# Performance work log

Measured on AMD Instinct MI355X. Metric: run time of the kernel, lower is better.

The kernel has to match this reference:

```python
import jax, jax.numpy as jnp
import numpy as np

L, D, H, B, S, V = 4, 1024, 16, 8, 512, 32000
DK = D // H          # per-head dim = 64; only head 0 is ever used (bug in source)
FF = 4 * D
EPS = 1e-3           # keras BatchNormalization default epsilon


def _bn(x, gamma, beta, mean, var):
    # inference-mode BatchNorm over last axis (keras default)
    return gamma * (x - mean) * jax.lax.rsqrt(var + EPS) + beta


def setup_inputs() -> dict:
    key = jax.random.key(0)
    keys = iter(jax.random.split(key, 40))

    def rn(shape, scale=0.02):
        return jax.random.normal(next(keys), shape, jnp.float32) * scale

    sequence = jax.random.randint(next(keys), (B, S), 0, V, dtype=jnp.int32)

    # standard sinusoidal positional encoding table [S, D]
    pos = np.arange(S)[:, None].astype(np.float32)
    i = np.arange(D)[None, :]
    angle = pos / np.power(10000.0, (2 * (i // 2)) / D).astype(np.float32)
    pes = np.where(i % 2 == 0, np.sin(angle), np.cos(angle)).astype(np.float32)

    return {
        "sequence": sequence,
        "emb": rn((V, D)),
        "pes": jnp.asarray(pes),
        # single-head attention params (head 0 only, per the source bug), stacked over layers
        "wq": rn((L, D, DK)), "bq": jnp.zeros((L, DK)),
        "wk": rn((L, D, DK)), "bk": jnp.zeros((L, DK)),
        "wv": rn((L, D, DK)), "bv": jnp.zeros((L, DK)),
        "wo": rn((L, DK, D)), "bo": jnp.zeros((L, D)),
        "att_gamma": 1.0 + rn((L, D), 0.1), "att_beta": rn((L, D), 0.1),
        "att_mean": rn((L, D), 0.1), "att_var": jnp.ones((L, D)),
        "w1": rn((L, D, FF)), "bff1": jnp.zeros((L, FF)),
        "w2": rn((L, FF, D)), "bff2": jnp.zeros((L, D)),
        "ffn_gamma": 1.0 + rn((L, D), 0.1), "ffn_beta": rn((L, D), 0.1),
        "ffn_mean": rn((L, D), 0.1), "ffn_var": jnp.ones((L, D)),
    }


def reference(sequence, emb, pes, wq, bq, wk, bk, wv, bv, wo, bo,
              att_gamma, att_beta, att_mean, att_var,
              w1, bff1, w2, bff2,
              ffn_gamma, ffn_beta, ffn_mean, ffn_var):
    # embedding + positional bug: only pes[i, 0] (a scalar per position) is added
    x = emb[sequence] + pes[:S, 0:1][None]          # [B, S, D]
    scale = 1.0 / jnp.sqrt(jnp.float32(DK))
    for l in range(L):
        q = x @ wq[l] + bq[l]                       # [B, S, DK]
        k = x @ wk[l] + bk[l]
        v = x @ wv[l] + bv[l]
        score = jnp.einsum('bqd,bkd->bqk', q, k) * scale
        head = jax.nn.softmax(score, axis=-1) @ v   # [B, S, DK]
        att = head @ wo[l] + bo[l]                  # [B, S, D]
        x = _bn(x + att, att_gamma[l], att_beta[l], att_mean[l], att_var[l])
        ffn = jax.nn.relu(x @ w1[l] + bff1[l]) @ w2[l] + bff2[l]
        x = _bn(x + ffn, ffn_gamma[l], ffn_beta[l], ffn_mean[l], ffn_var[l])
    return x
```

## Files before the change

### kernel.cpp

```cpp
#include <hip/hip_runtime.h>
#include <hip/hip_bf16.h>
#include <stdint.h>

#define L_  4
#define D_  1024
#define DK_ 64
#define B_  8
#define S_  512
#define FF_ 4096
#define M_  (B_*S_)
#define EPS_ 1e-3f
#define QKVN_ 256

typedef __bf16 bf16_t;
typedef bf16_t bf16x8 __attribute__((ext_vector_type(8)));
typedef float  f32x4  __attribute__((ext_vector_type(4)));

__device__ __forceinline__ bf16_t f2b(float f) {
    union { float f; uint32_t u; } v; v.f = f;
    uint32_t r = v.u + 0x7fff + ((v.u >> 16) & 1);
    uint16_t h = (uint16_t)(r >> 16);
    bf16_t o; __builtin_memcpy(&o, &h, 2); return o;
}

__device__ __forceinline__ void gl2lds16(const bf16_t* g, bf16_t* l) {
    __builtin_amdgcn_global_load_lds(
        (__attribute__((address_space(1))) void*)g,
        (__attribute__((address_space(3))) void*)l, 16, 0, 0);
}

__global__ void embed_kernel(const int* __restrict__ seq, const float* __restrict__ emb,
                             const float* __restrict__ pes, float* __restrict__ x,
                             bf16_t* __restrict__ xb) {
    int idx = blockIdx.x * 256 + threadIdx.x;
    int md  = idx >> 10;
    int d   = idx & (D_ - 1);
    int s   = md & (S_ - 1);
    float v = emb[(size_t)seq[md] * D_ + d] + pes[s * D_];
    x[idx] = v;
    xb[idx] = f2b(v);
}

__device__ __forceinline__ void tile_tr(const float* __restrict__ src, bf16_t* __restrict__ dst,
                                        int K, int N, int kb, int nb, float (*t)[33]) {
    int k0 = kb * 32, n0 = nb * 32;
    int c = threadIdx.x & 31, r = threadIdx.x >> 5;
    #pragma unroll
    for (int i = 0; i < 4; i++)
        t[r + i * 8][c] = src[(size_t)(k0 + r + i * 8) * N + n0 + c];
    __syncthreads();
    #pragma unroll
    for (int i = 0; i < 4; i++)
        dst[(size_t)(n0 + r + i * 8) * K + k0 + c] = f2b(t[c][r + i * 8]);
}

__global__ void prep_weights(const float* __restrict__ wq, const float* __restrict__ wk,
                             const float* __restrict__ wv, const float* __restrict__ wo,
                             const float* __restrict__ w1, const float* __restrict__ w2,
                             const float* __restrict__ bq, const float* __restrict__ bk,
                             const float* __restrict__ bv,
                             bf16_t* __restrict__ wqkvt, bf16_t* __restrict__ wot,
                             bf16_t* __restrict__ w1t, bf16_t* __restrict__ w2t,
                             float* __restrict__ bqkv) {
    __shared__ float t[32][33];
    int bid = blockIdx.x;
    if (bid < 4096) {
        tile_tr(w1, w1t, D_, FF_, bid & 31, bid >> 5, t);
    } else if (bid < 8192) {
        int rem = bid - 4096;
        tile_tr(w2, w2t, FF_, D_, rem & 127, rem >> 7, t);
    } else if (bid < 8384) {
        int rem = bid - 8192;
        int which = rem >> 6; rem &= 63;
        const float* src = which == 0 ? wq : (which == 1 ? wk : wv);
        tile_tr(src, wqkvt + (size_t)which * 64 * D_, D_, DK_, rem & 31, rem >> 5, t);
    } else if (bid < 8448) {
        int rem = bid - 8384;
        tile_tr(wo, wot, DK_, D_, rem & 1, rem >> 1, t);
    } else if (bid < 8464) {
        int rem = bid - 8448;
        bf16_t* z = wqkvt + (size_t)192 * D_ + rem * 4096;
        for (int i = threadIdx.x; i < 4096; i += 256) z[i] = (bf16_t)0.f;
    } else {
        int n = threadIdx.x;
        float v = 0.f;
        if      (n <  64) v = bq[n];
        else if (n < 128) v = bk[n - 64];
        else if (n < 192) v = bv[n - 128];
        bqkv[n] = v;
    }
}

template<int MODE>
__global__ __launch_bounds__(256)
void gemm_mfma3(const bf16_t* __restrict__ A, const bf16_t* __restrict__ Bt,
                const float* __restrict__ bias, bf16_t* __restrict__ Cb,
                const float* __restrict__ Xin, float* __restrict__ Xf, bf16_t* __restrict__ Xb,
                const float* __restrict__ g, const float* __restrict__ bb,
                const float* __restrict__ mu, const float* __restrict__ var,
                int N, int K, int kChunk, size_t strideZ) {
    __shared__ bf16_t As[128 * 64];
    __shared__ bf16_t Bs[128 * 64];
    const int tid  = threadIdx.x;
    const int w    = tid >> 6, lane = tid & 63;
    const int wm   = w >> 1,   wn   = w & 1;
    const int lm   = lane & 15, quad = lane >> 4;
    const int m0 = blockIdx.y * 128, n0 = blockIdx.x * 128;
    const int kBeg = blockIdx.z * kChunk, kEnd = kBeg + kChunk;
    const int lrow = lane >> 3;
    const int lk   = (lane & 7) ^ lrow;

    f32x4 acc[4][4];
    #pragma unroll
    for (int i = 0; i < 4; i++)
        #pragma unroll
        for (int j = 0; j < 4; j++) acc[i][j] = (f32x4){0.f, 0.f, 0.f, 0.f};

    for (int k0 = kBeg; k0 < kEnd; k0 += 64) {
        #pragma unroll
        for (int i = 0; i < 4; i++) {
            const int r0 = w * 32 + i * 8;
            gl2lds16(A  + (size_t)(m0 + r0 + lrow) * K + k0 + lk * 8, As + r0 * 64);
            gl2lds16(Bt + (size_t)(n0 + r0 + lrow) * K + k0 + lk * 8, Bs + r0 * 64);
        }
        __syncthreads();
        #pragma unroll
        for (int s = 0; s < 2; s++) {
            bf16x8 af[4], bfr[4];
            #pragma unroll
            for (int mi = 0; mi < 4; mi++) {
                const int ra = wm * 64 + mi * 16 + lm;
                af[mi] = *(const bf16x8*)(As + ra * 64 + (((s * 4 + quad) ^ (lm & 7)) * 8));
            }
            #pragma unroll
            for (int ni = 0; ni < 4; ni++) {
                const int rb = wn * 64 + ni * 16 + lm;
                bfr[ni] = *(const bf16x8*)(Bs + rb * 64 + (((s * 4 + quad) ^ (lm & 7)) * 8));
            }
            #pragma unroll
            for (int mi = 0; mi < 4; mi++)
                #pragma unroll
                for (int ni = 0; ni < 4; ni++)
                    acc[mi][ni] = __builtin_amdgcn_mfma_f32_16x16x32_bf16(
                        af[mi], bfr[ni], acc[mi][ni], 0, 0, 0);
        }
        __syncthreads();
    }

    bf16_t* Pz = (MODE == 2) ? Cb + (size_t)blockIdx.z * strideZ : Cb;

    #pragma unroll
    for (int ni = 0; ni < 4; ni++) {
        const int col = n0 + wn * 64 + ni * 16 + lm;
        float bv = 0.f, gv = 0.f, bbv = 0.f, muv = 0.f, rsv = 0.f;
        if (MODE != 2) bv = bias[col];
        if (MODE == 3) {
            gv = g[col]; bbv = bb[col]; muv = mu[col];
            rsv = rsqrtf(var[col] + EPS_);
        }
        #pragma unroll
        for (int mi = 0; mi < 4; mi++) {
            const int rbase = m0 + wm * 64 + mi * 16 + quad * 4;
            #pragma unroll
            for (int r = 0; r < 4; r++) {
                const size_t idx = (size_t)(rbase + r) * N + col;
                float v = acc[mi][ni][r] + bv;
                if (MODE == 2) Pz[idx] = f2b(v);
                if (MODE == 3) {
                    float s = Xin[idx] + v;
                    float o = gv * (s - muv) * rsv + bbv;
                    Xf[idx] = o;
                    Xb[idx] = f2b(o);
                }
            }
        }
    }
}

template<int MODE>
__global__ __launch_bounds__(512, 2)
void gemm_8ph(const bf16_t* __restrict__ A, const bf16_t* __restrict__ Bt,
              const float* __restrict__ bias, bf16_t* __restrict__ Cb,
              int N, int K, int kChunk, size_t strideZ) {
    __shared__ bf16_t As[2][256 * 64];
    __shared__ bf16_t Bs[2][256 * 64];
    const int tid  = threadIdx.x;
    const int w    = tid >> 6, lane = tid & 63;
    const int wm   = w >> 2,   wn   = w & 3;
    const int lm   = lane & 15, quad = lane >> 4;
    const int m0 = blockIdx.y * 256, n0 = blockIdx.x * 256;
    const int kBeg = blockIdx.z * kChunk;
    const int lrow = lane >> 3;
    const int lk   = (lane & 7) ^ lrow;
    const int niter = kChunk >> 7;

    f32x4 acc[8][4];
    #pragma unroll
    for (int i = 0; i < 8; i++)
        #pragma unroll
        for (int j = 0; j < 4; j++) acc[i][j] = (f32x4){0.f, 0.f, 0.f, 0.f};

    auto stageA = [&](int buf, int half, int tile) {
        const int kt0 = kBeg + tile * 64;
        #pragma unroll
        for (int j = 0; j < 2; j++) {
            const int r0 = half * 128 + w * 16 + j * 8;
            gl2lds16(A + (size_t)(m0 + r0 + lrow) * K + kt0 + lk * 8, &As[buf][r0 * 64]);
        }
    };
    auto stageB = [&](int buf, int half, int tile) {
        const int kt0 = kBeg + tile * 64;
        #pragma unroll
        for (int j = 0; j < 2; j++) {
            const int r0 = half * 128 + w * 16 + j * 8;
            gl2lds16(Bt + (size_t)(n0 + r0 + lrow) * K + kt0 + lk * 8, &Bs[buf][r0 * 64]);
        }
    };

    bf16x8 af[8], bfr[4];
    auto ldFrags = [&](int buf, int kk) {
        #pragma unroll
        for (int mi = 0; mi < 8; mi++) {
            const int ra = wm * 128 + mi * 16 + lm;
            af[mi] = *(const bf16x8*)(&As[buf][ra * 64 + (((kk * 4 + quad) ^ (lm & 7)) * 8)]);
        }
        #pragma unroll
        for (int ni = 0; ni < 4; ni++) {
            const int rb = wn * 64 + ni * 16 + lm;
            bfr[ni] = *(const bf16x8*)(&Bs[buf][rb * 64 + (((kk * 4 + quad) ^ (lm & 7)) * 8)]);
        }
    };
    auto mfmaHalf = [&](int mh) {
        __builtin_amdgcn_s_setprio(1);
        #pragma unroll
        for (int mi = mh * 4; mi < mh * 4 + 4; mi++)
            #pragma unroll
            for (int ni = 0; ni < 4; ni++)
                acc[mi][ni] = __builtin_amdgcn_mfma_f32_16x16x32_bf16(
                    af[mi], bfr[ni], acc[mi][ni], 0, 0, 0);
        __builtin_amdgcn_s_setprio(0);
    };

    stageA(0, 0, 0); stageA(0, 1, 0); stageB(0, 0, 0); stageB(0, 1, 0);
    stageA(1, 0, 1);
    asm volatile("s_waitcnt vmcnt(2)" ::: "memory");
    __builtin_amdgcn_sched_barrier(0);
    __builtin_amdgcn_s_barrier();

    for (int i = 0; i < niter; i++) {
        const int t0 = 2 * i;
        const bool nl = (i < niter - 1);
        ldFrags(0, 0);
        stageA(1, 1, t0 + 1);
        __builtin_amdgcn_s_barrier();
        mfmaHalf(0);
        __builtin_amdgcn_s_barrier();
        stageB(1, 0, t0 + 1);
        __builtin_amdgcn_s_barrier();
        mfmaHalf(1);
        __builtin_amdgcn_s_barrier();
        ldFrags(0, 1);
        stageB(1, 1, t0 + 1);
        __builtin_amdgcn_s_barrier();
        mfmaHalf(0);
        __builtin_amdgcn_s_barrier();
        if (nl) {
            stageA(0, 0, t0 + 2);
            asm volatile("s_waitcnt vmcnt(2)" ::: "memory");
        } else {
            asm volatile("s_waitcnt vmcnt(0)" ::: "memory");
        }
        __builtin_amdgcn_sched_barrier(0);
        __builtin_amdgcn_s_barrier();
        mfmaHalf(1);
        __builtin_amdgcn_s_barrier();
        ldFrags(1, 0);
        if (nl) stageA(0, 1, t0 + 2);
        __builtin_amdgcn_s_barrier();
        mfmaHalf(0);
        __builtin_amdgcn_s_barrier();
        if (nl) stageB(0, 0, t0 + 2);
        __builtin_amdgcn_s_barrier();
        mfmaHalf(1);
        __builtin_amdgcn_s_barrier();
        ldFrags(1, 1);
        if (nl) stageB(0, 1, t0 + 2);
        __builtin_amdgcn_s_barrier();
        mfmaHalf(0);
        __builtin_amdgcn_s_barrier();
        if (nl) {
            stageA(1, 0, t0 + 3);
            asm volatile("s_waitcnt vmcnt(2)" ::: "memory");
        } else {
            asm volatile("s_waitcnt vmcnt(0)" ::: "memory");
        }
        __builtin_amdgcn_sched_barrier(0);
        __builtin_amdgcn_s_barrier();
        mfmaHalf(1);
        __builtin_amdgcn_s_barrier();
    }

    bf16_t* Pz = (MODE == 2) ? Cb + (size_t)blockIdx.z * strideZ : Cb;

    #pragma unroll
    for (int ni = 0; ni < 4; ni++) {
        const int col = n0 + wn * 64 + ni * 16 + lm;
        float bv = 0.f;
        if (MODE == 1) bv = bias[col];
        #pragma unroll
        for (int mi = 0; mi < 8; mi++) {
            const int rbase = m0 + wm * 128 + mi * 16 + quad * 4;
            #pragma unroll
            for (int r = 0; r < 4; r++) {
                const size_t idx = (size_t)(rbase + r) * N + col;
                float v = acc[mi][ni][r] + bv;
                if (MODE == 1) Cb[idx] = f2b(fmaxf(v, 0.f));
                if (MODE == 2) Pz[idx] = f2b(v);
            }
        }
    }
}

__global__ void qkv_reduce(const bf16_t* __restrict__ P, const float* __restrict__ bias,
                           bf16_t* __restrict__ dst) {
    int idx = blockIdx.x * 256 + threadIdx.x;
    int n = idx & (QKVN_ - 1);
    float s = bias[n];
    #pragma unroll
    for (int zz = 0; zz < 4; zz++) s += (float)P[(size_t)zz * M_ * QKVN_ + idx];
    dst[idx] = f2b(s);
}

__global__ void vt_kernel(const bf16_t* __restrict__ qkv, bf16_t* __restrict__ Vt) {
    int b = blockIdx.y, k0 = blockIdx.x * 64;
    const bf16_t* vb = qkv + (size_t)b * S_ * QKVN_ + 128;
    __shared__ bf16_t t[64][65];
    int c = threadIdx.x & 63, r4 = threadIdx.x >> 6;
    #pragma unroll
    for (int i = 0; i < 16; i++) {
        int k = i * 4 + r4;
        t[c][k] = vb[(size_t)(k0 + k) * QKVN_ + c];
    }
    __syncthreads();
    #pragma unroll
    for (int i = 0; i < 16; i++) {
        int d = i * 4 + r4;
        Vt[((size_t)b * DK_ + d) * S_ + k0 + c] = t[d][c];
    }
}

__global__ __launch_bounds__(256)
void attn_fused(const bf16_t* __restrict__ qkv, const bf16_t* __restrict__ Vt,
                bf16_t* __restrict__ hdb) {
    const int b  = blockIdx.y;
    const int i0 = blockIdx.x * 64;
    const bf16_t* qb  = qkv + (size_t)b * S_ * QKVN_;
    const bf16_t* kb  = qb + 64;
    const bf16_t* vtb = Vt + (size_t)b * DK_ * S_;

    __shared__ bf16_t Ps[8 * 64 * 64];
    __shared__ bf16_t Vs[8 * 64 * 64];
    __shared__ float  rowred[4][64];

    const int tid  = threadIdx.x;
    const int w    = tid >> 6, lane = tid & 63;
    const int lm   = lane & 15, quad = lane >> 4;
    const int lrow = lane >> 3;
    const int lk   = (lane & 7) ^ lrow;

    #pragma unroll
    for (int i = 0; i < 16; i++) {
        const int r0 = w * 16 + (i & 1) * 8;
        const int kt = i >> 1;
        gl2lds16(vtb + (size_t)(r0 + lrow) * S_ + kt * 64 + lk * 8,
                 Vs + kt * 4096 + r0 * 64);
    }

    f32x4 acc[4][8];
    #pragma unroll
    for (int mi = 0; mi < 4; mi++)
        #pragma unroll
        for (int ni = 0; ni < 8; ni++) acc[mi][ni] = (f32x4){0.f, 0.f, 0.f, 0.f};

    #pragma unroll
    for (int s = 0; s < 2; s++) {
        bf16x8 af[4], bfr[8];
        #pragma unroll
        for (int mi = 0; mi < 4; mi++)
            af[mi] = *(const bf16x8*)(qb + (size_t)(i0 + mi * 16 + lm) * QKVN_ + s * 32 + quad * 8);
        #pragma unroll
        for (int ni = 0; ni < 8; ni++)
            bfr[ni] = *(const bf16x8*)(kb + (size_t)(w * 128 + ni * 16 + lm) * QKVN_ + s * 32 + quad * 8);
        #pragma unroll
        for (int mi = 0; mi < 4; mi++)
            #pragma unroll
            for (int ni = 0; ni < 8; ni++)
                acc[mi][ni] = __builtin_amdgcn_mfma_f32_16x16x32_bf16(
                    af[mi], bfr[ni], acc[mi][ni], 0, 0, 0);
    }
    #pragma unroll
    for (int mi = 0; mi < 4; mi++)
        #pragma unroll
        for (int ni = 0; ni < 8; ni++) acc[mi][ni] *= 0.125f;

    float rmax[4][4];
    #pragma unroll
    for (int mi = 0; mi < 4; mi++)
        #pragma unroll
        for (int r = 0; r < 4; r++) {
            float m = acc[mi][0][r];
            #pragma unroll
            for (int ni = 1; ni < 8; ni++) m = fmaxf(m, acc[mi][ni][r]);
            #pragma unroll
            for (int off = 1; off < 16; off <<= 1) m = fmaxf(m, __shfl_xor(m, off, 64));
            rmax[mi][r] = m;
        }
    if (lm == 0) {
        #pragma unroll
        for (int mi = 0; mi < 4; mi++)
            #pragma unroll
            for (int r = 0; r < 4; r++)
                rowred[w][mi * 16 + quad * 4 + r] = rmax[mi][r];
    }
    __syncthreads();
    float gmax[4][4];
    #pragma unroll
    for (int mi = 0; mi < 4; mi++)
        #pragma unroll
        for (int r = 0; r < 4; r++) {
            const int row = mi * 16 + quad * 4 + r;
            gmax[mi][r] = fmaxf(fmaxf(rowred[0][row], rowred[1][row]),
                                fmaxf(rowred[2][row], rowred[3][row]));
        }
    __syncthreads();

    float rsum[4][4];
    #pragma unroll
    for (int mi = 0; mi < 4; mi++)
        #pragma unroll
        for (int r = 0; r < 4; r++) rsum[mi][r] = 0.f;
    #pragma unroll
    for (int mi = 0; mi < 4; mi++) {
        #pragma unroll
        for (int ni = 0; ni < 8; ni++) {
            const int key = w * 128 + ni * 16 + lm;
            const int kt  = key >> 6;
            const int ck  = (key >> 3) & 7;
            #pragma unroll
            for (int r = 0; r < 4; r++) {
                const int m = mi * 16 + quad * 4 + r;
                float p = __expf(acc[mi][ni][r] - gmax[mi][r]);
                bf16_t pb = f2b(p);
                rsum[mi][r] += (float)pb;
                Ps[kt * 4096 + m * 64 + ((ck ^ (m & 7)) * 8) + (key & 7)] = pb;
            }
        }
    }
    #pragma unroll
    for (int mi = 0; mi < 4; mi++)
        #pragma unroll
        for (int r = 0; r < 4; r++) {
            float s = rsum[mi][r];
            #pragma unroll
            for (int off = 1; off < 16; off <<= 1) s += __shfl_xor(s, off, 64);
            rsum[mi][r] = s;
        }
    if (lm == 0) {
        #pragma unroll
        for (int mi = 0; mi < 4; mi++)
            #pragma unroll
            for (int r = 0; r < 4; r++)
                rowred[w][mi * 16 + quad * 4 + r] = rsum[mi][r];
    }
    __syncthreads();

    f32x4 accO[4];
    #pragma unroll
    for (int ni = 0; ni < 4; ni++) accO[ni] = (f32x4){0.f, 0.f, 0.f, 0.f};
    #pragma unroll
    for (int ks = 0; ks < 16; ks++) {
        const int kt = ks >> 1;
        const int co = (ks & 1) * 4 + quad;
        bf16x8 af = *(const bf16x8*)(Ps + kt * 4096 + (w * 16 + lm) * 64 + ((co ^ (lm & 7)) * 8));
        #pragma unroll
        for (int ni = 0; ni < 4; ni++) {
            bf16x8 bfr = *(const bf16x8*)(Vs + kt * 4096 + (ni * 16 + lm) * 64 + ((co ^ (lm & 7)) * 8));
            accO[ni] = __builtin_amdgcn_mfma_f32_16x16x32_bf16(af, bfr, accO[ni], 0, 0, 0);
        }
    }

    #pragma unroll
    for (int r = 0; r < 4; r++) {
        const int row = w * 16 + quad * 4 + r;
        const float tot = rowred[0][row] + rowred[1][row] + rowred[2][row] + rowred[3][row];
        const float inv = 1.0f / tot;
        #pragma unroll
        for (int ni = 0; ni < 4; ni++)
            hdb[(size_t)(b * S_ + i0 + row) * DK_ + ni * 16 + lm] = f2b(accO[ni][r] * inv);
    }
}

__global__ void bn_residual4(const float* __restrict__ x, const bf16_t* __restrict__ p,
                             const float* __restrict__ bias,
                             const float* __restrict__ g, const float* __restrict__ b,
                             const float* __restrict__ mu, const float* __restrict__ var,
                             float* __restrict__ dst, bf16_t* __restrict__ dstb) {
    int idx = blockIdx.x * 256 + threadIdx.x;
    int d = idx & (D_ - 1);
    float r = bias[d] + (float)p[idx] + (float)p[(size_t)M_ * D_ + idx]
            + (float)p[2 * (size_t)M_ * D_ + idx] + (float)p[3 * (size_t)M_ * D_ + idx];
    float s = x[idx] + r;
    float o = g[d] * (s - mu[d]) * rsqrtf(var[d] + EPS_) + b[d];
    dst[idx] = o;
    dstb[idx] = f2b(o);
}

extern "C" void kernel_launch(void* const* d_in, const int* in_sizes, int n_in,
                              void* d_out, int out_size, void* d_ws, size_t ws_size,
                              hipStream_t stream) {
    const int*   seq = (const int*)  d_in[0];
    const float* emb = (const float*)d_in[1];
    const float* pes = (const float*)d_in[2];
    const float* wq  = (const float*)d_in[3];
    const float* bq  = (const float*)d_in[4];
    const float* wk  = (const float*)d_in[5];
    const float* bk  = (const float*)d_in[6];
    const float* wv  = (const float*)d_in[7];
    const float* bv  = (const float*)d_in[8];
    const float* wo  = (const float*)d_in[9];
    const float* bo  = (const float*)d_in[10];
    const float* ag  = (const float*)d_in[11];
    const float* ab  = (const float*)d_in[12];
    const float* am  = (const float*)d_in[13];
    const float* av  = (const float*)d_in[14];
    const float* w1  = (const float*)d_in[15];
    const float* b1  = (const float*)d_in[16];
    const float* w2  = (const float*)d_in[17];
    const float* b2  = (const float*)d_in[18];
    const float* fg  = (const float*)d_in[19];
    const float* fb  = (const float*)d_in[20];
    const float* fm  = (const float*)d_in[21];
    const float* fv  = (const float*)d_in[22];
    float* out = (float*)d_out;

    char* p = (char*)d_ws;
    auto alloc = [&](size_t bytes) { char* q = p; p += (bytes + 255) & ~(size_t)255; return q; };
    float*  X     = (float*) alloc((size_t)M_ * D_ * 4);
    bf16_t* Xb    = (bf16_t*)alloc((size_t)M_ * D_ * 2);
    bf16_t* qkvb  = (bf16_t*)alloc((size_t)M_ * QKVN_ * 2);
    bf16_t* Vtb   = (bf16_t*)alloc((size_t)B_ * DK_ * S_ * 2);
    bf16_t* hdb   = (bf16_t*)alloc((size_t)M_ * DK_ * 2);
    bf16_t* hb    = (bf16_t*)alloc((size_t)M_ * FF_ * 2);
    bf16_t* w1t   = (bf16_t*)alloc((size_t)FF_ * D_ * 2);
    bf16_t* w2t   = (bf16_t*)alloc((size_t)D_ * FF_ * 2);
    bf16_t* wqkvt = (bf16_t*)alloc((size_t)QKVN_ * D_ * 2);
    bf16_t* wot   = (bf16_t*)alloc((size_t)D_ * DK_ * 2);
    bf16_t* part  = (bf16_t*)alloc((size_t)4 * M_ * D_ * 2);
    float*  bqkv  = (float*) alloc(QKVN_ * 4);

    embed_kernel<<<M_ * D_ / 256, 256, 0, stream>>>(seq, emb, pes, X, Xb);

    for (int l = 0; l < L_; l++) {
        prep_weights<<<8465, 256, 0, stream>>>(
            wq + (size_t)l * D_ * DK_, wk + (size_t)l * D_ * DK_, wv + (size_t)l * D_ * DK_,
            wo + (size_t)l * DK_ * D_, w1 + (size_t)l * D_ * FF_, w2 + (size_t)l * FF_ * D_,
            bq + l * DK_, bk + l * DK_, bv + l * DK_,
            wqkvt, wot, w1t, w2t, bqkv);

        gemm_mfma3<2><<<dim3(QKVN_ / 128, M_ / 128, 4), 256, 0, stream>>>(
            Xb, wqkvt, nullptr, (bf16_t*)out, nullptr, nullptr, nullptr,
            nullptr, nullptr, nullptr, nullptr, QKVN_, D_, D_ / 4, (size_t)M_ * QKVN_);
        qkv_reduce<<<M_ * QKVN_ / 256, 256, 0, stream>>>((const bf16_t*)out, bqkv, qkvb);

        vt_kernel<<<dim3(S_ / 64, B_), 256, 0, stream>>>(qkvb, Vtb);
        attn_fused<<<dim3(S_ / 64, B_), 256, 0, stream>>>(qkvb, Vtb, hdb);

        gemm_mfma3<3><<<dim3(D_ / 128, M_ / 128, 1), 256, 0, stream>>>(
            hdb, wot, bo + l * D_, nullptr, X, X, Xb,
            ag + l * D_, ab + l * D_, am + l * D_, av + l * D_, D_, DK_, DK_, 0);

        gemm_8ph<1><<<dim3(FF_ / 256, M_ / 256, 1), 512, 0, stream>>>(
            Xb, w1t, b1 + l * FF_, hb, FF_, D_, D_, 0);

        gemm_8ph<2><<<dim3(D_ / 256, M_ / 256, 4), 512, 0, stream>>>(
            hb, w2t, nullptr, part, D_, FF_, FF_ / 4, (size_t)M_ * D_);

        bn_residual4<<<M_ * D_ / 256, 256, 0, stream>>>(
            X, part, b2 + l * D_,
            fg + l * D_, fb + l * D_, fm + l * D_, fv + l * D_, X, Xb);
        if (l == L_ - 1)
            hipMemcpyAsync(out, X, (size_t)M_ * D_ * 4, hipMemcpyDeviceToDevice, stream);
    }
}
```

Baseline: 934.7 us.

## Replace 8-phase GEMM pipeline with 4-stage K32 ring buffer and XCD-aware block remap

The FFN GEMMs drop the hand-interleaved 8-phase schedule with double-buffered K=64 tiles. They now use a 4-deep ring of K=32 LDS tiles, prefetching three tiles ahead with a single barrier per k-step and a different XOR swizzle. Workgroup IDs are also remapped round-robin across the 8 XCDs to improve L2 locality. This trades the finer-grained overlap of loads and MFMAs for deeper prefetch and fewer barriers, but each k-step does less MFMA work per barrier.

New measurement: 989.7 us. +5.9%, slower.

```diff
diff --git a/kernel.cpp b/kernel.cpp
--- a/kernel.cpp
+++ b/kernel.cpp
@@ -179,20 +179,25 @@
 
 template<int MODE>
 __global__ __launch_bounds__(512, 2)
-void gemm_8ph(const bf16_t* __restrict__ A, const bf16_t* __restrict__ Bt,
-              const float* __restrict__ bias, bf16_t* __restrict__ Cb,
-              int N, int K, int kChunk, size_t strideZ) {
-    __shared__ bf16_t As[2][256 * 64];
-    __shared__ bf16_t Bs[2][256 * 64];
+void gemm_ring(const bf16_t* __restrict__ A, const bf16_t* __restrict__ Bt,
+               const float* __restrict__ bias, bf16_t* __restrict__ Cb,
+               int N, int K, int kChunk, size_t strideZ) {
+    __shared__ bf16_t As[4][256 * 32];
+    __shared__ bf16_t Bs[4][256 * 32];
     const int tid  = threadIdx.x;
     const int w    = tid >> 6, lane = tid & 63;
     const int wm   = w >> 2,   wn   = w & 3;
     const int lm   = lane & 15, quad = lane >> 4;
-    const int m0 = blockIdx.y * 256, n0 = blockIdx.x * 256;
+
+    const int nwg = gridDim.x * gridDim.y;
+    int wg = blockIdx.y * gridDim.x + blockIdx.x;
+    wg = (wg & 7) * (nwg >> 3) + (wg >> 3);
+    const int m0 = (wg / gridDim.x) * 256, n0 = (wg % gridDim.x) * 256;
+
     const int kBeg = blockIdx.z * kChunk;
-    const int lrow = lane >> 3;
-    const int lk   = (lane & 7) ^ lrow;
-    const int niter = kChunk >> 7;
+    const int nkt  = kChunk >> 5;
+    const int lrow = lane >> 2;
+    const int lk   = (lane & 3) ^ ((lane >> 3) & 3);
 
     f32x4 acc[8][4];
     #pragma unroll
@@ -200,103 +205,65 @@
         #pragma unroll
         for (int j = 0; j < 4; j++) acc[i][j] = (f32x4){0.f, 0.f, 0.f, 0.f};
 
-    auto stageA = [&](int buf, int half, int tile) {
-        const int kt0 = kBeg + tile * 64;
+    auto stage = [&](const bf16_t* __restrict__ src, int base, int tile, bf16_t* dst) {
+        const int kt0 = kBeg + tile * 32;
         #pragma unroll
         for (int j = 0; j < 2; j++) {
-            const int r0 = half * 128 + w * 16 + j * 8;
-            gl2lds16(A + (size_t)(m0 + r0 + lrow) * K + kt0 + lk * 8, &As[buf][r0 * 64]);
+            const int r0 = w * 32 + j * 16;
+            gl2lds16(src + (size_t)(base + r0 + lrow) * K + kt0 + lk * 8, dst + r0 * 32);
         }
     };
-    auto stageB = [&](int buf, int half, int tile) {
-        const int kt0 = kBeg + tile * 64;
-        #pragma unroll
-        for (int j = 0; j < 2; j++) {
-            const int r0 = half * 128 + w * 16 + j * 8;
-            gl2lds16(Bt + (size_t)(n0 + r0 + lrow) * K + kt0 + lk * 8, &Bs[buf][r0 * 64]);
-        }
-    };
-
-    bf16x8 af[8], bfr[4];
-    auto ldFrags = [&](int buf, int kk) {
-        #pragma unroll
-        for (int mi = 0; mi < 8; mi++) {
+
+    #pragma unroll
+    for (int t = 0; t < 3; t++) {
+        stage(A,  m0, t, As[t]);
+        stage(Bt, n0, t, Bs[t]);
+    }
+
+    for (int kt = 0; kt < nkt; ++kt) {
+        const int buf = kt & 3;
+        if (kt + 3 < nkt) {
+            const int sb = (kt + 3) & 3;
+            stage(A,  m0, kt + 3, As[sb]);
+            stage(Bt, n0, kt + 3, Bs[sb]);
+            asm volatile("s_waitcnt vmcnt(12)" ::: "memory");
+        } else if (kt + 3 == nkt) {
+            asm volatile("s_waitcnt vmcnt(8)" ::: "memory");
+        } else if (kt + 2 == nkt) {
+            asm volatile("s_waitcnt vmcnt(4)" ::: "memory");
+        } else {
+            asm volatile("s_waitcnt vmcnt(0)" ::: "memory");
+        }
+        __builtin_amdgcn_sched_barrier(0);
+        __builtin_amdgcn_s_barrier();
+        __builtin_amdgcn_sched_barrier(0);
+
+        bf16x8 af[8], bfr[4];
+        #pragma unroll
+        for (int mi = 0; mi < 4; mi++) {
             const int ra = wm * 128 + mi * 16 + lm;
-            af[mi] = *(const bf16x8*)(&As[buf][ra * 64 + (((kk * 4 + quad) ^ (lm & 7)) * 8)]);
+            af[mi] = *(const bf16x8*)(&As[buf][ra * 32 + ((quad ^ ((ra >> 1) & 3)) * 8)]);
         }
         #pragma unroll
         for (int ni = 0; ni < 4; ni++) {
             const int rb = wn * 64 + ni * 16 + lm;
-            bfr[ni] = *(const bf16x8*)(&Bs[buf][rb * 64 + (((kk * 4 + quad) ^ (lm & 7)) * 8)]);
-        }
-    };
-    auto mfmaHalf = [&](int mh) {
+            bfr[ni] = *(const bf16x8*)(&Bs[buf][rb * 32 + ((quad ^ ((rb >> 1) & 3)) * 8)]);
+        }
+        #pragma unroll
+        for (int mi = 4; mi < 8; mi++) {
+            const int ra = wm * 128 + mi * 16 + lm;
+            af[mi] = *(const bf16x8*)(&As[buf][ra * 32 + ((quad ^ ((ra >> 1) & 3)) * 8)]);
+        }
+
         __builtin_amdgcn_s_setprio(1);
         #pragma unroll
-        for (int mi = mh * 4; mi < mh * 4 + 4; mi++)
+        for (int mi = 0; mi < 8; mi++)
             #pragma unroll
             for (int ni = 0; ni < 4; ni++)
                 acc[mi][ni] = __builtin_amdgcn_mfma_f32_16x16x32_bf16(
                     af[mi], bfr[ni], acc[mi][ni], 0, 0, 0);
         __builtin_amdgcn_s_setprio(0);
-    };
-
-    stageA(0, 0, 0); stageA(0, 1, 0); stageB(0, 0, 0); stageB(0, 1, 0);
-    stageA(1, 0, 1);
-    asm volatile("s_waitcnt vmcnt(2)" ::: "memory");
-    __builtin_amdgcn_sched_barrier(0);
-    __builtin_amdgcn_s_barrier();
-
-    for (int i = 0; i < niter; i++) {
-        const int t0 = 2 * i;
-        const bool nl = (i < niter - 1);
-        ldFrags(0, 0);
-        stageA(1, 1, t0 + 1);
-        __builtin_amdgcn_s_barrier();
-        mfmaHalf(0);
-        __builtin_amdgcn_s_barrier();
-        stageB(1, 0, t0 + 1);
-        __builtin_amdgcn_s_barrier();
-        mfmaHalf(1);
-        __builtin_amdgcn_s_barrier();
-        ldFrags(0, 1);
-        stageB(1, 1, t0 + 1);
-        __builtin_amdgcn_s_barrier();
-        mfmaHalf(0);
-        __builtin_amdgcn_s_barrier();
-        if (nl) {
-            stageA(0, 0, t0 + 2);
-            asm volatile("s_waitcnt vmcnt(2)" ::: "memory");
-        } else {
-            asm volatile("s_waitcnt vmcnt(0)" ::: "memory");
-        }
-        __builtin_amdgcn_sched_barrier(0);
-        __builtin_amdgcn_s_barrier();
-        mfmaHalf(1);
-        __builtin_amdgcn_s_barrier();
-        ldFrags(1, 0);
-        if (nl) stageA(0, 1, t0 + 2);
-        __builtin_amdgcn_s_barrier();
-        mfmaHalf(0);
-        __builtin_amdgcn_s_barrier();
-        if (nl) stageB(0, 0, t0 + 2);
-        __builtin_amdgcn_s_barrier();
-        mfmaHalf(1);
-        __builtin_amdgcn_s_barrier();
-        ldFrags(1, 1);
-        if (nl) stageB(0, 1, t0 + 2);
-        __builtin_amdgcn_s_barrier();
-        mfmaHalf(0);
-        __builtin_amdgcn_s_barrier();
-        if (nl) {
-            stageA(1, 0, t0 + 3);
-            asm volatile("s_waitcnt vmcnt(2)" ::: "memory");
-        } else {
-            asm volatile("s_waitcnt vmcnt(0)" ::: "memory");
-        }
-        __builtin_amdgcn_sched_barrier(0);
-        __builtin_amdgcn_s_barrier();
-        mfmaHalf(1);
+
         __builtin_amdgcn_s_barrier();
     }
 
@@ -579,10 +546,10 @@
             hdb, wot, bo + l * D_, nullptr, X, X, Xb,
             ag + l * D_, ab + l * D_, am + l * D_, av + l * D_, D_, DK_, DK_, 0);
 
-        gemm_8ph<1><<<dim3(FF_ / 256, M_ / 256, 1), 512, 0, stream>>>(
+        gemm_ring<1><<<dim3(FF_ / 256, M_ / 256, 1), 512, 0, stream>>>(
             Xb, w1t, b1 + l * FF_, hb, FF_, D_, D_, 0);
 
-        gemm_8ph<2><<<dim3(D_ / 256, M_ / 256, 4), 512, 0, stream>>>(
+        gemm_ring<2><<<dim3(D_ / 256, M_ / 256, 4), 512, 0, stream>>>(
             hb, w2t, nullptr, part, D_, FF_, FF_ / 4, (size_t)M_ * D_);
 
         bn_residual4<<<M_ * D_ / 256, 256, 0, stream>>>(
```
